# Performance work log

Hardware: AMD Instinct MI355X
Metric: run time of the kernel (lower is better)

Reference implementation:

```python
import jax, jax.numpy as jnp
import numpy as np

N_T, N_I = 4096, 4096
TEXT_DIM, IMAGE_DIM, HIDDEN_DIM = 1024, 1024, 1024


def setup_inputs() -> dict:
    key = jax.random.key(0)
    ks = jax.random.split(key, 8)
    s_t = 1.0 / np.sqrt(TEXT_DIM)
    s_i = 1.0 / np.sqrt(IMAGE_DIM)
    return {
        "text_features": jax.random.normal(ks[0], (N_T, TEXT_DIM), jnp.float32),
        "image_features": jax.random.normal(ks[1], (N_I, IMAGE_DIM), jnp.float32),
        # nn.Linear params: weight [out, in], bias [out]
        "w_text": jax.random.uniform(ks[2], (HIDDEN_DIM, TEXT_DIM), jnp.float32, -s_t, s_t),
        "b_text": jax.random.uniform(ks[3], (HIDDEN_DIM,), jnp.float32, -s_t, s_t),
        "w_image": jax.random.uniform(ks[4], (HIDDEN_DIM, IMAGE_DIM), jnp.float32, -s_i, s_i),
        "b_image": jax.random.uniform(ks[5], (HIDDEN_DIM,), jnp.float32, -s_i, s_i),
        "scale_TI": jnp.ones((1,), jnp.float32),
        "scale_IT": jnp.ones((1,), jnp.float32),
    }


def reference(text_features, image_features, w_text, b_text, w_image, b_image, scale_TI, scale_IT):
    # linear projections to shared hidden space
    t = text_features @ w_text.T + b_text      # [N_t, H]
    i = image_features @ w_image.T + b_image   # [N_i, H]
    inv_sqrt_h = 1.0 / jnp.sqrt(jnp.asarray(HIDDEN_DIM, t.dtype))
    # text -> image attention: softmax over image axis, scaled post-softmax
    logits_TI = (t @ i.T) * inv_sqrt_h               # [N_t, N_i]
    attn_TI = jax.nn.softmax(logits_TI, axis=-1) * scale_TI
    # image -> text attention
    attn_IT = jax.nn.softmax(logits_TI.T, axis=-1) * scale_IT  # [N_i, N_t]
    text_attention_on_image = attn_TI @ image_features  # [N_t, image_dim]
    image_attention_on_text = attn_IT @ text_features   # [N_i, text_dim]
    return (text_attention_on_image, image_attention_on_text)
```

## Files before the change

kernel.cpp:

```cpp
#include <hip/hip_runtime.h>


typedef __bf16 bf16x8 __attribute__((ext_vector_type(8)));
typedef float f32x4 __attribute__((ext_vector_type(4)));

#define N_T 4096
#define N_I 4096
#define DIM 1024
#define TSS 136

__device__ __forceinline__ unsigned short f2bf(float f) {
    unsigned int u = __float_as_uint(f);
    u += 0x7fffu + ((u >> 16) & 1u);
    return (unsigned short)(u >> 16);
}

__device__ __forceinline__ void async_cp16(const unsigned short* g, unsigned short* l) {
    __builtin_amdgcn_global_load_lds(
        (const __attribute__((address_space(1))) unsigned int*)g,
        (__attribute__((address_space(3))) unsigned int*)l, 16, 0, 0);
}

__device__ __forceinline__ void stage_async(const unsigned short* __restrict__ src,
                                            int ld, int row0, int k0,
                                            unsigned short* lds, int t) {
    int r = t >> 2, c = (t & 3) << 3;
    const unsigned short* g = src + (size_t)(row0 + r) * ld + k0 + c;
    async_cp16(g, lds + r * 32 + c);
    async_cp16(g + (size_t)64 * ld, lds + (64 + r) * 32 + c);
}

__device__ __forceinline__ void stage_async64(const unsigned short* __restrict__ src,
                                              int ld, int row0, int k0,
                                              unsigned short* lds, int t) {
    int r = t >> 2, c = (t & 3) << 3;
    async_cp16(src + (size_t)(row0 + r) * ld + k0 + c, lds + r * 32 + c);
}

__device__ __forceinline__ void mfma_step(const unsigned short* As,
                                          const unsigned short* Bs, f32x4 acc[4][4],
                                          int wrow, int wcol, int lane16, int quad) {
    bf16x8 a[4], b[4];
#pragma unroll
    for (int i = 0; i < 4; ++i) {
        a[i] = *(const bf16x8*)&As[(wrow + i * 16 + lane16) * 32 + quad * 8];
        b[i] = *(const bf16x8*)&Bs[(wcol + i * 16 + lane16) * 32 + quad * 8];
    }
#pragma unroll
    for (int i = 0; i < 4; ++i)
#pragma unroll
        for (int j = 0; j < 4; ++j)
            acc[i][j] = __builtin_amdgcn_mfma_f32_16x16x32_bf16(a[i], b[j], acc[i][j], 0, 0, 0);
}

__device__ __forceinline__ void mfma_step42(const unsigned short* As,
                                            const unsigned short* Bs, f32x4 acc[4][2],
                                            int wrow, int wcol, int lane16, int quad) {
    bf16x8 a[4], b[2];
#pragma unroll
    for (int i = 0; i < 4; ++i)
        a[i] = *(const bf16x8*)&As[(wrow + i * 16 + lane16) * 32 + quad * 8];
#pragma unroll
    for (int j = 0; j < 2; ++j)
        b[j] = *(const bf16x8*)&Bs[(wcol + j * 16 + lane16) * 32 + quad * 8];
#pragma unroll
    for (int i = 0; i < 4; ++i)
#pragma unroll
        for (int j = 0; j < 2; ++j)
            acc[i][j] = __builtin_amdgcn_mfma_f32_16x16x32_bf16(a[i], b[j], acc[i][j], 0, 0, 0);
}

__device__ __forceinline__ void tile_store(const unsigned short* sm,
                                           unsigned short* __restrict__ g, int ld,
                                           int row0, int col0, int tid) {
    int r = tid >> 1, h = (tid & 1) << 6;
    const unsigned short* src = sm + r * TSS + h;
    unsigned short* dst = g + (size_t)(row0 + r) * ld + col0 + h;
#pragma unroll
    for (int v = 0; v < 8; ++v)
        *(uint4*)(dst + v * 8) = *(const uint4*)(src + v * 8);
}

__global__ void __launch_bounds__(256)
cvt_all(const float* __restrict__ im, const float* __restrict__ tx,
        const float* __restrict__ wt, const float* __restrict__ wi,
        unsigned short* __restrict__ imb, unsigned short* __restrict__ txb,
        unsigned short* __restrict__ imgT, unsigned short* __restrict__ textT,
        unsigned short* __restrict__ wtb, unsigned short* __restrict__ wib,
        float* __restrict__ lTI) {
    int t = threadIdx.x;
    if (blockIdx.z == 2) {
        int lin = blockIdx.y * 64 + blockIdx.x;
        if (lin < 4) {
            *(f32x4*)&lTI[(lin * 256 + t) * 8] = (f32x4){0.f, 0.f, 0.f, 0.f};
            *(f32x4*)&lTI[(lin * 256 + t) * 8 + 4] = (f32x4){0.f, 0.f, 0.f, 0.f};
        }
        size_t i = (size_t)(lin * 256 + t) * 8;
        const float* s;
        unsigned short* d;
        size_t off;
        if (i < 1048576) { s = wt; d = wtb; off = i; }
        else             { s = wi; d = wib; off = i - 1048576; }
        float4 f0 = *(const float4*)(s + off);
        float4 f1 = *(const float4*)(s + off + 4);
        uint4 o;
        o.x = (unsigned int)f2bf(f0.x) | ((unsigned int)f2bf(f0.y) << 16);
        o.y = (unsigned int)f2bf(f0.z) | ((unsigned int)f2bf(f0.w) << 16);
        o.z = (unsigned int)f2bf(f1.x) | ((unsigned int)f2bf(f1.y) << 16);
        o.w = (unsigned int)f2bf(f1.z) | ((unsigned int)f2bf(f1.w) << 16);
        *(uint4*)(d + off) = o;
        return;
    }
    const float* in = blockIdx.z ? tx : im;
    unsigned short* nb = blockIdx.z ? txb : imb;
    unsigned short* tr = blockIdx.z ? textT : imgT;
    __shared__ float tile[64][65];
    int row0 = blockIdx.x * 64, col0 = blockIdx.y * 64;
    int r = t >> 2, c = (t & 3) << 4;
    {
        const float* p = in + (size_t)(row0 + r) * DIM + col0 + c;
        float4 f0 = *(const float4*)(p);
        float4 f1 = *(const float4*)(p + 4);
        float4 f2 = *(const float4*)(p + 8);
        float4 f3 = *(const float4*)(p + 12);
        *(float4*)&tile[r][c] = f0;
        *(float4*)&tile[r][c + 4] = f1;
        *(float4*)&tile[r][c + 8] = f2;
        *(float4*)&tile[r][c + 12] = f3;
        uint4 o0, o1;
        o0.x = (unsigned int)f2bf(f0.x) | ((unsigned int)f2bf(f0.y) << 16);
        o0.y = (unsigned int)f2bf(f0.z) | ((unsigned int)f2bf(f0.w) << 16);
        o0.z = (unsigned int)f2bf(f1.x) | ((unsigned int)f2bf(f1.y) << 16);
        o0.w = (unsigned int)f2bf(f1.z) | ((unsigned int)f2bf(f1.w) << 16);
        o1.x = (unsigned int)f2bf(f2.x) | ((unsigned int)f2bf(f2.y) << 16);
        o1.y = (unsigned int)f2bf(f2.z) | ((unsigned int)f2bf(f2.w) << 16);
        o1.z = (unsigned int)f2bf(f3.x) | ((unsigned int)f2bf(f3.y) << 16);
        o1.w = (unsigned int)f2bf(f3.z) | ((unsigned int)f2bf(f3.w) << 16);
        unsigned short* q = nb + (size_t)(row0 + r) * DIM + col0 + c;
        *(uint4*)q = o0;
        *(uint4*)(q + 8) = o1;
    }
    __syncthreads();
    {
        unsigned short v[16];
#pragma unroll
        for (int u = 0; u < 16; ++u) v[u] = f2bf(tile[c + u][r]);
        unsigned short* q = tr + (size_t)(col0 + r) * N_T + row0 + c;
        *(uint4*)q = *(uint4*)&v[0];
        *(uint4*)(q + 8) = *(uint4*)&v[8];
    }
}

__global__ void __launch_bounds__(256, 4)
gemm_proj2(const unsigned short* __restrict__ Atx, const unsigned short* __restrict__ Wtx,
           const float* __restrict__ btx, unsigned short* __restrict__ Ctx,
           const unsigned short* __restrict__ Aim, const unsigned short* __restrict__ Wim,
           const float* __restrict__ bim, unsigned short* __restrict__ Cim) {
    __shared__ unsigned short As[2][128 * 32];
    __shared__ unsigned short Bs[2][64 * 32];
    int z = blockIdx.z;
    const unsigned short* A = z ? Aim : Atx;
    const unsigned short* W = z ? Wim : Wtx;
    const float* bias = z ? bim : btx;
    unsigned short* C = z ? Cim : Ctx;
    int tid = threadIdx.x;
    int m0 = blockIdx.x * 128, n0 = blockIdx.y * 64;
    int lane = tid & 63, wave = tid >> 6;
    int lane16 = lane & 15, quad = lane >> 4;
    int wrow = (wave >> 1) * 64, wcol = (wave & 1) * 32;
    f32x4 acc[4][2];
    {
        f32x4 zz = {0.f, 0.f, 0.f, 0.f};
        for (int i = 0; i < 4; ++i)
            for (int j = 0; j < 2; ++j) acc[i][j] = zz;
    }
    for (int k0 = 0; k0 < DIM; k0 += 64) {
        stage_async(A, DIM, m0, k0, As[0], tid);
        stage_async64(W, DIM, n0, k0, Bs[0], tid);
        stage_async(A, DIM, m0, k0 + 32, As[1], tid);
        stage_async64(W, DIM, n0, k0 + 32, Bs[1], tid);
        __syncthreads();
        mfma_step42(As[0], Bs[0], acc, wrow, wcol, lane16, quad);
        mfma_step42(As[1], Bs[1], acc, wrow, wcol, lane16, quad);
        __syncthreads();
    }
#pragma unroll
    for (int j = 0; j < 2; ++j) {
        int col = n0 + wcol + j * 16 + lane16;
        float bv = bias[col];
#pragma unroll
        for (int i = 0; i < 4; ++i) {
            int rowb = m0 + wrow + i * 16 + quad * 4;
#pragma unroll
            for (int r = 0; r < 4; ++r)
                C[(size_t)(rowb + r) * DIM + col] = f2bf(acc[i][j][r] + bv);
        }
    }
}

__global__ void __launch_bounds__(256, 4)
gemm_logits_exp(const unsigned short* __restrict__ Tb,
                const unsigned short* __restrict__ Ib,
                unsigned short* __restrict__ P, unsigned short* __restrict__ PT,
                float* __restrict__ lT, float* __restrict__ lI) {
    __shared__ unsigned short smem[128 * TSS];
    unsigned short* As0 = smem;
    unsigned short* Bs0 = smem + 4096;
    unsigned short* As1 = smem + 8192;
    unsigned short* Bs1 = smem + 12288;
    float* lred = (float*)(smem + 16384);
    float* cred = lred + 128;
    int tid = threadIdx.x;
    int m0 = blockIdx.x * 128, n0 = blockIdx.y * 128;
    int lane = tid & 63, wave = tid >> 6;
    int lane16 = lane & 15, quad = lane >> 4;
    int wrow = (wave >> 1) * 64, wcol = (wave & 1) * 64;
    f32x4 acc[4][4];
    {
        f32x4 z = {0.f, 0.f, 0.f, 0.f};
        for (int i = 0; i < 4; ++i)
            for (int j = 0; j < 4; ++j) acc[i][j] = z;
    }
    for (int k0 = 0; k0 < DIM; k0 += 64) {
        stage_async(Tb, DIM, m0, k0, As0, tid);
        stage_async(Ib, DIM, n0, k0, Bs0, tid);
        stage_async(Tb, DIM, m0, k0 + 32, As1, tid);
        stage_async(Ib, DIM, n0, k0 + 32, Bs1, tid);
        __syncthreads();
        mfma_step(As0, Bs0, acc, wrow, wcol, lane16, quad);
        mfma_step(As1, Bs1, acc, wrow, wcol, lane16, quad);
        __syncthreads();
    }
#pragma unroll
    for (int i = 0; i < 4; ++i)
#pragma unroll
        for (int j = 0; j < 4; ++j)
#pragma unroll
            for (int r = 0; r < 4; ++r)
                acc[i][j][r] = __expf(acc[i][j][r] * 0.03125f);
    float rs[4][4];
#pragma unroll
    for (int i = 0; i < 4; ++i)
#pragma unroll
        for (int r = 0; r < 4; ++r) {
            float s = acc[i][0][r] + acc[i][1][r] + acc[i][2][r] + acc[i][3][r];
            s += __shfl_xor(s, 1); s += __shfl_xor(s, 2);
            s += __shfl_xor(s, 4); s += __shfl_xor(s, 8);
            rs[i][r] = s;
        }
    float cs[4];
#pragma unroll
    for (int j = 0; j < 4; ++j) {
        float s = 0.f;
#pragma unroll
        for (int i = 0; i < 4; ++i)
#pragma unroll
            for (int r = 0; r < 4; ++r) s += acc[i][j][r];
        s += __shfl_xor(s, 16); s += __shfl_xor(s, 32);
        cs[j] = s;
    }
    if (wave & 1) {
        if (lane16 == 0)
#pragma unroll
            for (int i = 0; i < 4; ++i)
#pragma unroll
                for (int r = 0; r < 4; ++r)
                    lred[wrow + i * 16 + quad * 4 + r] = rs[i][r];
    }
    if (wave >> 1) {
        if (quad == 0)
#pragma unroll
            for (int j = 0; j < 4; ++j)
                cred[wcol + j * 16 + lane16] = cs[j];
    }
    __syncthreads();
    if (!(wave & 1) && lane16 == 0) {
#pragma unroll
        for (int i = 0; i < 4; ++i)
#pragma unroll
            for (int r = 0; r < 4; ++r) {
                int row = wrow + i * 16 + quad * 4 + r;
                atomicAdd(&lT[m0 + row], rs[i][r] + lred[row]);
            }
    }
    if (!(wave >> 1) && quad == 0) {
#pragma unroll
        for (int j = 0; j < 4; ++j) {
            int col = wcol + j * 16 + lane16;
            atomicAdd(&lI[n0 + col], cs[j] + cred[col]);
        }
    }
    __syncthreads();
#pragma unroll
    for (int i = 0; i < 4; ++i)
#pragma unroll
        for (int j = 0; j < 4; ++j)
#pragma unroll
            for (int r = 0; r < 4; ++r)
                smem[(wrow + i * 16 + quad * 4 + r) * TSS + wcol + j * 16 + lane16] =
                    f2bf(acc[i][j][r]);
    __syncthreads();
    tile_store(smem, P, N_I, m0, n0, tid);
    __syncthreads();
#pragma unroll
    for (int i = 0; i < 4; ++i)
#pragma unroll
        for (int j = 0; j < 4; ++j) {
            unsigned int lo = (unsigned int)f2bf(acc[i][j][0]) |
                              ((unsigned int)f2bf(acc[i][j][1]) << 16);
            unsigned int hi = (unsigned int)f2bf(acc[i][j][2]) |
                              ((unsigned int)f2bf(acc[i][j][3]) << 16);
            uint2 v; v.x = lo; v.y = hi;
            *(uint2*)&smem[(wcol + j * 16 + lane16) * TSS + wrow + i * 16 + quad * 4] = v;
        }
    __syncthreads();
    tile_store(smem, PT, N_T, n0, m0, tid);
}

__global__ void __launch_bounds__(512, 4)
gemm_attn2(const unsigned short* __restrict__ P, const unsigned short* __restrict__ imgT,
           const float* __restrict__ lT, const float* __restrict__ sTI,
           float* __restrict__ out0,
           const unsigned short* __restrict__ PT, const unsigned short* __restrict__ textT,
           const float* __restrict__ lI, const float* __restrict__ sIT,
           float* __restrict__ out1) {
    __shared__ unsigned short As[2][2][128 * 32];
    __shared__ unsigned short Bs[2][2][128 * 32];
    int which = blockIdx.z;
    const unsigned short* A = which ? PT : P;
    const unsigned short* Bt = which ? textT : imgT;
    const float* l = which ? lI : lT;
    const float* sp = which ? sIT : sTI;
    float* out = which ? out1 : out0;

    int tid = threadIdx.x;
    int half = tid >> 8;
    int t = tid & 255;
    int m0 = blockIdx.x * 128, n0 = blockIdx.y * 128;
    int lane = tid & 63;
    int wv = (tid >> 6) & 3;
    int lane16 = lane & 15, quad = lane >> 4;
    int wrow = (wv >> 1) * 64, wcol = (wv & 1) * 64;
    f32x4 acc[4][4];
    {
        f32x4 z = {0.f, 0.f, 0.f, 0.f};
        for (int i = 0; i < 4; ++i)
            for (int j = 0; j < 4; ++j) acc[i][j] = z;
    }

    int kbeg = half * 2048;
    for (int k0 = kbeg; k0 < kbeg + 2048; k0 += 64) {
        stage_async(A, 4096, m0, k0, As[half][0], t);
        stage_async(Bt, 4096, n0, k0, Bs[half][0], t);
        stage_async(A, 4096, m0, k0 + 32, As[half][1], t);
        stage_async(Bt, 4096, n0, k0 + 32, Bs[half][1], t);
        __syncthreads();
        mfma_step(As[half][0], Bs[half][0], acc, wrow, wcol, lane16, quad);
        mfma_step(As[half][1], Bs[half][1], acc, wrow, wcol, lane16, quad);
        __syncthreads();
    }

    float* red = (float*)As;
#pragma unroll
    for (int i = 0; i < 4; ++i) {
        __syncthreads();
        if (half) {
#pragma unroll
            for (int j = 0; j < 4; ++j)
                *(f32x4*)&red[wv * 1024 + lane * 16 + j * 4] = acc[i][j];
        }
        __syncthreads();
        if (!half) {
#pragma unroll
            for (int j = 0; j < 4; ++j)
                acc[i][j] += *(const f32x4*)&red[wv * 1024 + lane * 16 + j * 4];
        }
    }
    if (half) return;

    float sc = sp[0];
#pragma unroll
    for (int i = 0; i < 4; ++i) {
        int rowb = m0 + wrow + i * 16 + quad * 4;
        float fac[4];
#pragma unroll
        for (int r = 0; r < 4; ++r) fac[r] = sc / l[rowb + r];
#pragma unroll
        for (int j = 0; j < 4; ++j) {
            int col = n0 + wcol + j * 16 + lane16;
#pragma unroll
            for (int r = 0; r < 4; ++r)
                out[(size_t)(rowb + r) * DIM + col] = acc[i][j][r] * fac[r];
        }
    }
}

extern "C" void kernel_launch(void* const* d_in, const int* in_sizes, int n_in,
                              void* d_out, int out_size, void* d_ws, size_t ws_size,
                              hipStream_t stream) {
    const float* text = (const float*)d_in[0];
    const float* image = (const float*)d_in[1];
    const float* w_text = (const float*)d_in[2];
    const float* b_text = (const float*)d_in[3];
    const float* w_image = (const float*)d_in[4];
    const float* b_image = (const float*)d_in[5];
    const float* scale_TI = (const float*)d_in[6];
    const float* scale_IT = (const float*)d_in[7];
    float* out0 = (float*)d_out;
    float* out1 = out0 + (size_t)N_T * DIM;

    char* ws = (char*)d_ws;
    unsigned short* text_bf = (unsigned short*)(ws);
    unsigned short* image_bf = (unsigned short*)(ws + (8ull << 20));
    unsigned short* wt_bf = (unsigned short*)(ws + (16ull << 20));
    unsigned short* wi_bf = (unsigned short*)(ws + (18ull << 20));
    unsigned short* P = (unsigned short*)(ws);
    unsigned short* imgT = (unsigned short*)(ws + (32ull << 20));
    unsigned short* textT = (unsigned short*)(ws + (40ull << 20));
    unsigned short* t_bf = (unsigned short*)(ws + (48ull << 20));
    unsigned short* i_bf = (unsigned short*)(ws + (56ull << 20));
    unsigned short* PT = (unsigned short*)(ws + (64ull << 20));
    float* lT = (float*)(ws + (96ull << 20));
    float* lI = (float*)(ws + (96ull << 20) + 16384);

    cvt_all<<<dim3(N_T / 64, DIM / 64, 3), 256, 0, stream>>>(
        image, text, w_text, w_image, image_bf, text_bf, imgT, textT,
        wt_bf, wi_bf, lT);

    gemm_proj2<<<dim3(N_T / 128, DIM / 64, 2), 256, 0, stream>>>(
        text_bf, wt_bf, b_text, t_bf, image_bf, wi_bf, b_image, i_bf);

    gemm_logits_exp<<<dim3(N_T / 128, N_I / 128), 256, 0, stream>>>(t_bf, i_bf, P, PT, lT, lI);

    gemm_attn2<<<dim3(N_T / 128, DIM / 128, 2), 512, 0, stream>>>(
        P, imgT, lT, scale_TI, out0, PT, textT, lI, scale_IT, out1);
}
```

Baseline: 268.4 us.

## Rewrite attention-output GEMM with 256x128 tiles and triple-buffered async LDS pipeline

Replaces the split-K 128x128 attention GEMM, which needed a shared-memory reduction, with 256x128 tiles in which each of 8 waves owns a 64x64 sub-tile. The kernel uses a 3-slot dynamic-LDS ring fed by async global-to-LDS loads, overlapping loads for step s+2 with MFMA on step s via vmcnt waits. It adds an XOR swizzle on the LDS layout to avoid bank conflicts and raises priority around the MFMA bursts. It uses about 144KB of LDS per block and halves the number of blocks, which lowers occupancy.

```diff
diff --git a/kernel.cpp b/kernel.cpp
--- a/kernel.cpp
+++ b/kernel.cpp
@@ -8,6 +8,9 @@
 #define N_I 4096
 #define DIM 1024
 #define TSS 136
+
+#define AT_SLOT 24576
+#define AT_LDS_BYTES (3 * AT_SLOT * 2)
 
 __device__ __forceinline__ unsigned short f2bf(float f) {
     unsigned int u = __float_as_uint(f);
@@ -317,15 +320,60 @@
     tile_store(smem, PT, N_T, n0, m0, tid);
 }
 
-__global__ void __launch_bounds__(512, 4)
-gemm_attn2(const unsigned short* __restrict__ P, const unsigned short* __restrict__ imgT,
+
+__device__ __forceinline__ void at_stageA(const unsigned short* __restrict__ g,
+                                          int row0, int k0, unsigned short* lds, int t) {
+#pragma unroll
+    for (int u = 0; u < 4; ++u) {
+        int c = t + u * 512;
+        int r = c >> 3;
+        int kq = (c & 7) ^ (r & 7);
+        async_cp16(g + (size_t)(row0 + r) * 4096 + k0 + (kq << 3), lds + c * 8);
+    }
+}
+
+__device__ __forceinline__ void at_stageB(const unsigned short* __restrict__ g,
+                                          int row0, int k0, unsigned short* lds, int t) {
+#pragma unroll
+    for (int u = 0; u < 2; ++u) {
+        int c = t + u * 512;
+        int r = c >> 3;
+        int kq = (c & 7) ^ (r & 7);
+        async_cp16(g + (size_t)(row0 + r) * 4096 + k0 + (kq << 3), lds + c * 8);
+    }
+}
+
+__device__ __forceinline__ void at_phase(const unsigned short* As, const unsigned short* Bs,
+                                         f32x4 acc[4][4], int wrow, int wcol,
+                                         int lane16, int quad) {
+#pragma unroll
+    for (int ks = 0; ks < 2; ++ks) {
+        bf16x8 a[4], b[4];
+        int sw = (((ks << 2) | quad) ^ (lane16 & 7)) << 3;
+#pragma unroll
+        for (int i = 0; i < 4; ++i)
+            a[i] = *(const bf16x8*)&As[(wrow + i * 16 + lane16) * 64 + sw];
+#pragma unroll
+        for (int j = 0; j < 4; ++j)
+            b[j] = *(const bf16x8*)&Bs[(wcol + j * 16 + lane16) * 64 + sw];
+        __builtin_amdgcn_s_setprio(1);
+#pragma unroll
+        for (int i = 0; i < 4; ++i)
+#pragma unroll
+            for (int j = 0; j < 4; ++j)
+                acc[i][j] = __builtin_amdgcn_mfma_f32_16x16x32_bf16(a[i], b[j], acc[i][j], 0, 0, 0);
+        __builtin_amdgcn_s_setprio(0);
+    }
+}
+
+__global__ void __launch_bounds__(512)
+gemm_attn3(const unsigned short* __restrict__ P, const unsigned short* __restrict__ imgT,
            const float* __restrict__ lT, const float* __restrict__ sTI,
            float* __restrict__ out0,
            const unsigned short* __restrict__ PT, const unsigned short* __restrict__ textT,
            const float* __restrict__ lI, const float* __restrict__ sIT,
            float* __restrict__ out1) {
-    __shared__ unsigned short As[2][2][128 * 32];
-    __shared__ unsigned short Bs[2][2][128 * 32];
+    extern __shared__ unsigned short sm[];
     int which = blockIdx.z;
     const unsigned short* A = which ? PT : P;
     const unsigned short* Bt = which ? textT : imgT;
@@ -334,13 +382,10 @@
     float* out = which ? out1 : out0;
 
     int tid = threadIdx.x;
-    int half = tid >> 8;
-    int t = tid & 255;
-    int m0 = blockIdx.x * 128, n0 = blockIdx.y * 128;
-    int lane = tid & 63;
-    int wv = (tid >> 6) & 3;
+    int m0 = blockIdx.x * 256, n0 = blockIdx.y * 128;
+    int lane = tid & 63, wave = tid >> 6;
     int lane16 = lane & 15, quad = lane >> 4;
-    int wrow = (wv >> 1) * 64, wcol = (wv & 1) * 64;
+    int wrow = (wave >> 1) * 64, wcol = (wave & 1) * 64;
     f32x4 acc[4][4];
     {
         f32x4 z = {0.f, 0.f, 0.f, 0.f};
@@ -348,35 +393,38 @@
             for (int j = 0; j < 4; ++j) acc[i][j] = z;
     }
 
-    int kbeg = half * 2048;
-    for (int k0 = kbeg; k0 < kbeg + 2048; k0 += 64) {
-        stage_async(A, 4096, m0, k0, As[half][0], t);
-        stage_async(Bt, 4096, n0, k0, Bs[half][0], t);
-        stage_async(A, 4096, m0, k0 + 32, As[half][1], t);
-        stage_async(Bt, 4096, n0, k0 + 32, Bs[half][1], t);
-        __syncthreads();
-        mfma_step(As[half][0], Bs[half][0], acc, wrow, wcol, lane16, quad);
-        mfma_step(As[half][1], Bs[half][1], acc, wrow, wcol, lane16, quad);
-        __syncthreads();
-    }
-
-    float* red = (float*)As;
-#pragma unroll
-    for (int i = 0; i < 4; ++i) {
-        __syncthreads();
-        if (half) {
-#pragma unroll
-            for (int j = 0; j < 4; ++j)
-                *(f32x4*)&red[wv * 1024 + lane * 16 + j * 4] = acc[i][j];
-        }
-        __syncthreads();
-        if (!half) {
-#pragma unroll
-            for (int j = 0; j < 4; ++j)
-                acc[i][j] += *(const f32x4*)&red[wv * 1024 + lane * 16 + j * 4];
-        }
-    }
-    if (half) return;
+    at_stageA(A, m0, 0, sm, tid);
+    at_stageB(Bt, n0, 0, sm + 16384, tid);
+    at_stageA(A, m0, 64, sm + AT_SLOT, tid);
+    at_stageB(Bt, n0, 64, sm + AT_SLOT + 16384, tid);
+
+    int cur = 0;
+    for (int s = 0; s < 62; ++s) {
+        int ns = cur + 2; if (ns >= 3) ns -= 3;
+        unsigned short* nsl = sm + ns * AT_SLOT;
+        at_stageA(A, m0, (s + 2) * 64, nsl, tid);
+        at_stageB(Bt, n0, (s + 2) * 64, nsl + 16384, tid);
+        asm volatile("s_waitcnt vmcnt(12)" ::: "memory");
+        __builtin_amdgcn_s_barrier();
+        const unsigned short* cp = sm + cur * AT_SLOT;
+        at_phase(cp, cp + 16384, acc, wrow, wcol, lane16, quad);
+        asm volatile("s_waitcnt lgkmcnt(0)" ::: "memory");
+        __builtin_amdgcn_s_barrier();
+        cur += 1; if (cur >= 3) cur -= 3;
+    }
+    asm volatile("s_waitcnt vmcnt(6)" ::: "memory");
+    __builtin_amdgcn_s_barrier();
+    {
+        const unsigned short* cp = sm + cur * AT_SLOT;
+        at_phase(cp, cp + 16384, acc, wrow, wcol, lane16, quad);
+    }
+    cur += 1; if (cur >= 3) cur -= 3;
+    asm volatile("s_waitcnt vmcnt(0)" ::: "memory");
+    __builtin_amdgcn_s_barrier();
+    {
+        const unsigned short* cp = sm + cur * AT_SLOT;
+        at_phase(cp, cp + 16384, acc, wrow, wcol, lane16, quad);
+    }
 
     float sc = sp[0];
 #pragma unroll
@@ -423,6 +471,13 @@
     float* lT = (float*)(ws + (96ull << 20));
     float* lI = (float*)(ws + (96ull << 20) + 16384);
 
+    static bool lds_set = false;
+    if (!lds_set) {
+        hipFuncSetAttribute((const void*)gemm_attn3,
+                            hipFuncAttributeMaxDynamicSharedMemorySize, AT_LDS_BYTES);
+        lds_set = true;
+    }
+
     cvt_all<<<dim3(N_T / 64, DIM / 64, 3), 256, 0, stream>>>(
         image, text, w_text, w_image, image_bf, text_bf, imgT, textT,
         wt_bf, wi_bf, lT);
@@ -432,6 +487,6 @@
 
     gemm_logits_exp<<<dim3(N_T / 128, N_I / 128), 256, 0, stream>>>(t_bf, i_bf, P, PT, lT, lI);
 
-    gemm_attn2<<<dim3(N_T / 128, DIM / 128, 2), 512, 0, stream>>>(
+    gemm_attn3<<<dim3(N_T / 256, DIM / 128, 2), 512, AT_LDS_BYTES, stream>>>(
         P, imgT, lT, scale_TI, out0, PT, textT, lI, scale_IT, out1);
 }
```

Measured after the change: 261.1 us. 1.03x faster.
